# Kernel optimization log

Hardware: AMD Instinct MI355X
Metric: run time of the kernel (lower is better)

Reference implementation:

```python
import jax, jax.numpy as jnp
import numpy as np

N, E, F, H, C = 100000, 1600000, 128, 128, 40
NUM_LAYERS = 4
BN_EPS = 1e-5


def gcn_conv(x, src, dst, W, b, n):
    # PyG GCNConv with improved=True: self-loop edge weight 2.0
    e = src.shape[0]
    deg = jax.ops.segment_sum(jnp.ones((e,), x.dtype), dst, num_segments=n) + 2.0
    dinv = jnp.where(deg > 0, jax.lax.rsqrt(deg), 0.0)  # [n]
    xw = x @ W  # [n, out]
    coef = dinv[src] * dinv[dst]  # [e]
    agg = jax.ops.segment_sum(xw[src] * coef[:, None], dst, num_segments=n)
    agg = agg + (2.0 * dinv * dinv)[:, None] * xw  # self-loop term (weight 2)
    return agg + b


def batchnorm(x, gamma, beta):
    # training-mode BN (batch statistics, biased variance), eps=1e-5
    mu = jnp.mean(x, axis=0)
    var = jnp.mean(jnp.square(x - mu), axis=0)
    return (x - mu) * jax.lax.rsqrt(var + BN_EPS) * gamma + beta


def setup_inputs() -> dict:
    key = jax.random.key(0)
    ks = jax.random.split(key, 4)
    x = jax.random.normal(ks[0], (N, F), dtype=jnp.float32)
    edge_index = jax.random.randint(ks[1], (2, E), 0, N, dtype=jnp.int32)
    conv_w = jax.random.normal(ks[2], (NUM_LAYERS, F, H), dtype=jnp.float32) * 0.05
    conv_b = jnp.zeros((NUM_LAYERS, H), jnp.float32)
    bn_g = jnp.ones((NUM_LAYERS, H), jnp.float32)
    bn_b = jnp.zeros((NUM_LAYERS, H), jnp.float32)
    fc_w = jax.random.normal(ks[3], (NUM_LAYERS + 1, H, C), dtype=jnp.float32) * 0.05
    fc_b = jnp.zeros((NUM_LAYERS + 1, C), jnp.float32)
    return {"x": x, "edge_index": edge_index, "conv_w": conv_w, "conv_b": conv_b,
            "bn_g": bn_g, "bn_b": bn_b, "fc_w": fc_w, "fc_b": fc_b}


def reference(x, edge_index, conv_w, conv_b, bn_g, bn_b, fc_w, fc_b):
    n = x.shape[0]
    src, dst = edge_index[0], edge_index[1]
    outs = [x]
    h = x
    for i in range(NUM_LAYERS):
        h = gcn_conv(h, src, dst, conv_w[i], conv_b[i], n)
        h = batchnorm(h, bn_g[i], bn_b[i])
        h = jax.nn.relu(h)
        outs.append(h)
    # jumping-knowledge style sum of per-layer class heads (dropout = identity in eval)
    out = outs[0] @ fc_w[0] + fc_b[0]
    for i in range(1, NUM_LAYERS + 1):
        out = out + outs[i] @ fc_w[i] + fc_b[i]
    return jax.nn.log_softmax(out, axis=-1)
```

## Files before the change

kernel.cpp:

```cpp
#include <hip/hip_runtime.h>
#include <hip/hip_bf16.h>
#include <stdint.h>

#define NN 100000
#define NE 1600000
#define FD 128
#define CD 40
#define NL 4
#define NTB 391
#define TILE 4096
#define NTILES 391
#define EBCAP 8192
#define OCAP 5120

typedef __bf16 bf16;
typedef __bf16 bf16x8 __attribute__((ext_vector_type(8)));
typedef float f32x4 __attribute__((ext_vector_type(4)));

__device__ __forceinline__ unsigned short f2b(float f) {
  bf16 b = (bf16)f;
  unsigned short u;
  __builtin_memcpy(&u, &b, 2);
  return u;
}
__device__ __forceinline__ float lo16(unsigned int u) { return __uint_as_float(u << 16); }
__device__ __forceinline__ float hi16(unsigned int u) { return __uint_as_float(u & 0xffff0000u); }

__launch_bounds__(256)
__global__ void k_bfill(const int* __restrict__ src, const int* __restrict__ dst,
                        int* __restrict__ gcur, unsigned int* __restrict__ csrE) {
  __shared__ int cnt[NTB], pref[NTB], gofs[NTB];
  __shared__ int sc[512];
  __shared__ unsigned int stage[TILE];
  __shared__ unsigned short tgtb[TILE];
  int tid = threadIdx.x;
  int base = blockIdx.x * TILE;
  int tcnt = min(TILE, NE - base);
  for (int b = tid; b < NTB; b += 256) cnt[b] = 0;
  __syncthreads();
  unsigned int pay[16];
  int brk[16];
#pragma unroll
  for (int i = 0; i < 16; i++) {
    int e = base + tid + i * 256;
    if (e < NE) {
      int d = dst[e];
      int b = d >> 8;
      int r = atomicAdd(&cnt[b], 1);
      pay[i] = (unsigned int)src[e] | ((unsigned int)(d & 255) << 17);
      brk[i] = (b << 12) | r;
    } else {
      brk[i] = -1;
    }
  }
  __syncthreads();
  sc[tid] = (tid < NTB) ? cnt[tid] : 0;
  sc[tid + 256] = (tid + 256 < NTB) ? cnt[tid + 256] : 0;
  __syncthreads();
  for (int off = 1; off < 512; off <<= 1) {
    int a0 = (tid >= off) ? sc[tid - off] : 0;
    int a1 = sc[tid + 256 - off];
    __syncthreads();
    sc[tid] += a0;
    sc[tid + 256] += a1;
    __syncthreads();
  }
  for (int b = tid; b < NTB; b += 256) pref[b] = sc[b] - cnt[b];
  __syncthreads();
#pragma unroll
  for (int i = 0; i < 16; i++) {
    if (brk[i] >= 0) {
      int b = brk[i] >> 12, r = brk[i] & 4095;
      int p = pref[b] + r;
      if ((unsigned)p < (unsigned)TILE) {
        stage[p] = pay[i];
        tgtb[p] = (unsigned short)b;
      }
    }
  }
  for (int b = tid; b < NTB; b += 256) {
    int c = cnt[b];
    gofs[b] = c ? atomicAdd(&gcur[b], (c + 15) & ~15) : 0;
  }
  __syncthreads();
  for (int t = tid; t < tcnt; t += 256) {
    int b = tgtb[t];
    int pos = gofs[b] + (t - pref[b]);
    if ((unsigned)pos < (unsigned)EBCAP) csrE[(size_t)b * EBCAP + pos] = stage[t];
  }
  for (int b = tid; b < NTB; b += 256) {
    int c = cnt[b];
    if (c) {
      int pad = (c + 15) & ~15;
      for (int j = c; j < pad; j++) {
        int pos = gofs[b] + j;
        if ((unsigned)pos < (unsigned)EBCAP) csrE[(size_t)b * EBCAP + pos] = 0xFFFFFFFFu;
      }
    }
  }
}

__launch_bounds__(256)
__global__ void k_bsort(const int* __restrict__ gcur, const unsigned int* __restrict__ csrE,
                        unsigned int* __restrict__ csrp, float* __restrict__ dinv,
                        int2* __restrict__ rse) {
  __shared__ unsigned int ent[OCAP];
  __shared__ int c32[256], prefn[256], c2[256], sc[256];
  __shared__ int ecnt_s;
  int b = blockIdx.x, tid = threadIdx.x;
  c32[tid] = 0;
  c2[tid] = 0;
  if (tid == 0) ecnt_s = 0;
  __syncthreads();
  int claimed = min(gcur[b], EBCAP);
  const unsigned int* in = csrE + (size_t)b * EBCAP;
  for (int i = tid; i < claimed; i += 256) {
    unsigned int e = in[i];
    if (e != 0xFFFFFFFFu) {
      int idx = atomicAdd(&ecnt_s, 1);
      if (idx < OCAP) ent[idx] = e;
      atomicAdd(&c32[e >> 17], 1);
    }
  }
  __syncthreads();
  int cnt = min(ecnt_s, OCAP);
  int c = c32[tid];
  int pc = (c + 1) & ~1;
  sc[tid] = pc;
  __syncthreads();
  for (int off = 1; off < 256; off <<= 1) {
    int a = (tid >= off) ? sc[tid - off] : 0;
    __syncthreads();
    sc[tid] += a;
    __syncthreads();
  }
  prefn[tid] = sc[tid] - pc;
  int node = b * 256 + tid;
  if (node < NN) {
    dinv[node] = rsqrtf((float)c + 2.0f);
    int s = b * OCAP + prefn[tid];
    rse[node] = make_int2(s, s + pc);
  }
  if (c & 1) {
    int pos = prefn[tid] + c;
    if (pos < OCAP) csrp[b * OCAP + pos] = 0x1FFFFu;
  }
  __syncthreads();
  for (int i = tid; i < cnt; i += 256) {
    unsigned int e = ent[i];
    int dlo = e >> 17;
    int ofs = atomicAdd(&c2[dlo], 1);
    int pos = prefn[dlo] + ofs;
    if (pos < OCAP) csrp[b * OCAP + pos] = e & 0x1FFFFu;
  }
}

__global__ void k_pack(unsigned int* __restrict__ csrp, const float* __restrict__ dinv) {
  int i = blockIdx.x * 256 + threadIdx.x;
  unsigned int e = csrp[i];
  unsigned int s = e & 0x1FFFFu;
  unsigned int fix = 0;
  if (s < NN) {
    fix = (unsigned int)__float2uint_rn(dinv[s] * 32768.0f);
  } else {
    s = 0;
  }
  csrp[i] = (fix << 17) | s;
}

__global__ void k_repackall(const float* __restrict__ wc, const float* __restrict__ wf,
                            bf16* __restrict__ wp, bf16* __restrict__ wpfc) {
  int t = blockIdx.x * 256 + threadIdx.x;
  if (t < NL * 16384) {
    int j = t & 7, lane = (t >> 3) & 63, n0 = (t >> 9) & 7, k0 = (t >> 12) & 3, layer = t >> 14;
    int k = k0 * 32 + (lane >> 4) * 8 + j;
    int n = n0 * 16 + (lane & 15);
    wp[t] = (bf16)wc[(layer * 128 + k) * 128 + n];
    return;
  }
  t -= NL * 16384;
  if (t >= 5 * 6144) return;
  int j = t & 7, lane = (t >> 3) & 63;
  int rest = t >> 9;
  int n0 = rest % 3;
  int rest2 = rest / 3;
  int k0 = rest2 & 3, layer = rest2 >> 2;
  int k = k0 * 32 + (lane >> 4) * 8 + j;
  int n = n0 * 16 + (lane & 15);
  wpfc[t] = (n < CD) ? (bf16)wf[(layer * 128 + k) * CD + n] : (bf16)0.0f;
}

template <int NC, bool BN, bool INIT, bool LSM>
__launch_bounds__(256)
__global__ void k_gfc(const void* __restrict__ inp, const float* __restrict__ stats,
                      const float* __restrict__ g, const float* __restrict__ bb,
                      const bf16* __restrict__ wconv, const bf16* __restrict__ wfc,
                      const float* __restrict__ fcb, bf16* __restrict__ xwb,
                      float* __restrict__ out) {
  __shared__ bf16 wl[NC * 2048 + 6144];
  __shared__ float sc[128], sh[128];
  int tid = threadIdx.x;
  if (NC) {
    const uint4* gc = (const uint4*)wconv;
    uint4* lc = (uint4*)wl;
#pragma unroll
    for (int i = 0; i < NC; i++) lc[tid + i * 256] = gc[tid + i * 256];
  }
  {
    const uint4* gf = (const uint4*)wfc;
    uint4* lf = (uint4*)(wl + NC * 2048);
    for (int i = tid; i < 768; i += 256) lf[i] = gf[i];
  }
  if (BN && tid < 128) {
    const float invN = 1.0f / (float)NN;
    float s1 = stats[tid] + stats[256 + tid] + stats[512 + tid] + stats[768 + tid];
    float s2 = stats[128 + tid] + stats[384 + tid] + stats[640 + tid] + stats[896 + tid];
    float mu = s1 * invN;
    float var = s2 * invN - mu * mu;
    float s = g[tid] * rsqrtf(var + 1e-5f);
    sc[tid] = s;
    sh[tid] = bb[tid] - mu * s;
  }
  __syncthreads();
  int wid = tid >> 6, lane = tid & 63, quad = lane >> 4, l15 = lane & 15;
  int m_base = blockIdx.x * 64 + wid * 16;
  int arow = m_base + l15;
  if (arow >= NN) arow = NN - 1;
  f32x4 accc[NC > 0 ? NC : 1];
  f32x4 accf[3];
  if (NC) {
#pragma unroll
    for (int i = 0; i < NC; i++) accc[i] = (f32x4){0.f, 0.f, 0.f, 0.f};
  }
#pragma unroll
  for (int i = 0; i < 3; i++) accf[i] = (f32x4){0.f, 0.f, 0.f, 0.f};
#pragma unroll
  for (int k0 = 0; k0 < 4; k0++) {
    union Fr { bf16x8 v; unsigned short us[8]; } fr;
    if (BN) {
      const uint4* prow = (const uint4*)((const bf16*)inp + (size_t)arow * 128 + k0 * 32 + quad * 8);
      uint4 u = *prow;
      unsigned int uu[4] = {u.x, u.y, u.z, u.w};
      int kc = k0 * 32 + quad * 8;
#pragma unroll
      for (int p = 0; p < 4; p++) {
        float x0 = lo16(uu[p]) * sc[kc + 2 * p] + sh[kc + 2 * p];
        float x1 = hi16(uu[p]) * sc[kc + 2 * p + 1] + sh[kc + 2 * p + 1];
        fr.us[2 * p] = f2b(fmaxf(0.f, x0));
        fr.us[2 * p + 1] = f2b(fmaxf(0.f, x1));
      }
    } else {
      const float* prow = (const float*)inp + (size_t)arow * 128 + k0 * 32 + quad * 8;
      float4 u0 = *(const float4*)prow;
      float4 u1 = *(const float4*)(prow + 4);
      fr.us[0] = f2b(u0.x); fr.us[1] = f2b(u0.y); fr.us[2] = f2b(u0.z); fr.us[3] = f2b(u0.w);
      fr.us[4] = f2b(u1.x); fr.us[5] = f2b(u1.y); fr.us[6] = f2b(u1.z); fr.us[7] = f2b(u1.w);
    }
    bf16x8 a = fr.v;
    if (NC) {
#pragma unroll
      for (int n0 = 0; n0 < NC; n0++) {
        bf16x8 bfr = *reinterpret_cast<const bf16x8*>(&wl[(k0 * NC + n0) * 512 + lane * 8]);
        accc[n0] = __builtin_amdgcn_mfma_f32_16x16x32_bf16(a, bfr, accc[n0], 0, 0, 0);
      }
    }
#pragma unroll
    for (int n0 = 0; n0 < 3; n0++) {
      bf16x8 bfr = *reinterpret_cast<const bf16x8*>(&wl[NC * 2048 + (k0 * 3 + n0) * 512 + lane * 8]);
      accf[n0] = __builtin_amdgcn_mfma_f32_16x16x32_bf16(a, bfr, accf[n0], 0, 0, 0);
    }
  }
  int orow = m_base + quad * 4;
  if (NC) {
#pragma unroll
    for (int n0 = 0; n0 < NC; n0++) {
#pragma unroll
      for (int r2 = 0; r2 < 4; r2++) {
        int row = orow + r2;
        if (row < NN) xwb[(size_t)row * 128 + n0 * 16 + l15] = (bf16)accc[n0][r2];
      }
    }
  }
  if (!LSM) {
#pragma unroll
    for (int n0 = 0; n0 < 3; n0++) {
      int col = n0 * 16 + l15;
      if (col < CD) {
        float bias = fcb[col];
#pragma unroll
        for (int r2 = 0; r2 < 4; r2++) {
          int row = orow + r2;
          if (row < NN) {
            size_t idx = (size_t)row * CD + col;
            float v = accf[n0][r2] + bias;
            out[idx] = INIT ? v : out[idx] + v;
          }
        }
      }
    }
  } else {
    float bias[3];
#pragma unroll
    for (int n0 = 0; n0 < 3; n0++) {
      int col = n0 * 16 + l15;
      bias[n0] = (col < CD) ? fcb[col] : 0.f;
    }
#pragma unroll
    for (int r2 = 0; r2 < 4; r2++) {
      int row = orow + r2;
      float v[3];
#pragma unroll
      for (int n0 = 0; n0 < 3; n0++) {
        int col = n0 * 16 + l15;
        if (col < CD) {
          float prev = (row < NN) ? out[(size_t)row * CD + col] : 0.f;
          v[n0] = prev + accf[n0][r2] + bias[n0];
        } else {
          v[n0] = -1e30f;
        }
      }
      float m = fmaxf(v[0], fmaxf(v[1], v[2]));
#pragma unroll
      for (int s = 1; s < 16; s <<= 1) m = fmaxf(m, __shfl_xor(m, s, 64));
      float sum = 0.f;
#pragma unroll
      for (int n0 = 0; n0 < 3; n0++) {
        int col = n0 * 16 + l15;
        if (col < CD) sum += __expf(v[n0] - m);
      }
#pragma unroll
      for (int s = 1; s < 16; s <<= 1) sum += __shfl_xor(sum, s, 64);
      float ls = m + logf(sum);
      if (row < NN) {
#pragma unroll
        for (int n0 = 0; n0 < 3; n0++) {
          int col = n0 * 16 + l15;
          if (col < CD) out[(size_t)row * CD + col] = v[n0] - ls;
        }
      }
    }
  }
}

__launch_bounds__(256)
__global__ void k_gather(const uint2* __restrict__ xw, const int2* __restrict__ rse,
                         const unsigned int* __restrict__ csrp, const float* __restrict__ dinv,
                         uint2* __restrict__ aggb) {
  int tid = threadIdx.x;
  int n = blockIdx.x * 4 + (tid >> 6);
  int l = tid & 63;
  int h = l >> 5, cl = l & 31;
  float dn = dinv[n];
  float kk = dn * (1.0f / 32768.0f);
  uint2 u = xw[n * 32 + cl];
  float cs = (h == 0) ? 2.0f * dn * dn : 0.0f;
  float a0 = cs * lo16(u.x), a1 = cs * hi16(u.x);
  float a2 = cs * lo16(u.y), a3 = cs * hi16(u.y);
  int2 r = rse[n];
  int e = r.x, e1 = r.y;
  for (; e + 7 < e1; e += 8) {
    unsigned int p0 = csrp[e + h];
    unsigned int p1 = csrp[e + 2 + h];
    unsigned int p2 = csrp[e + 4 + h];
    unsigned int p3 = csrp[e + 6 + h];
    uint2 v0 = xw[(p0 & 0x1FFFFu) * 32 + cl];
    uint2 v1 = xw[(p1 & 0x1FFFFu) * 32 + cl];
    uint2 v2 = xw[(p2 & 0x1FFFFu) * 32 + cl];
    uint2 v3 = xw[(p3 & 0x1FFFFu) * 32 + cl];
    float c0 = (float)(p0 >> 17) * kk;
    float c1 = (float)(p1 >> 17) * kk;
    float c2 = (float)(p2 >> 17) * kk;
    float c3 = (float)(p3 >> 17) * kk;
    a0 += c0 * lo16(v0.x); a1 += c0 * hi16(v0.x); a2 += c0 * lo16(v0.y); a3 += c0 * hi16(v0.y);
    a0 += c1 * lo16(v1.x); a1 += c1 * hi16(v1.x); a2 += c1 * lo16(v1.y); a3 += c1 * hi16(v1.y);
    a0 += c2 * lo16(v2.x); a1 += c2 * hi16(v2.x); a2 += c2 * lo16(v2.y); a3 += c2 * hi16(v2.y);
    a0 += c3 * lo16(v3.x); a1 += c3 * hi16(v3.x); a2 += c3 * lo16(v3.y); a3 += c3 * hi16(v3.y);
  }
  for (; e + 1 < e1; e += 2) {
    unsigned int p0 = csrp[e + h];
    uint2 v0 = xw[(p0 & 0x1FFFFu) * 32 + cl];
    float c0 = (float)(p0 >> 17) * kk;
    a0 += c0 * lo16(v0.x); a1 += c0 * hi16(v0.x); a2 += c0 * lo16(v0.y); a3 += c0 * hi16(v0.y);
  }
  a0 += __shfl_xor(a0, 32, 64);
  a1 += __shfl_xor(a1, 32, 64);
  a2 += __shfl_xor(a2, 32, 64);
  a3 += __shfl_xor(a3, 32, 64);
  if (h == 0) {
    uint2 o;
    o.x = (unsigned int)f2b(a0) | ((unsigned int)f2b(a1) << 16);
    o.y = (unsigned int)f2b(a2) | ((unsigned int)f2b(a3) << 16);
    aggb[n * 32 + cl] = o;
  }
}

__launch_bounds__(256)
__global__ void k_stats(const uint2* __restrict__ agg, float* __restrict__ statsL) {
  __shared__ float ls1[128], ls2[128];
  int tid = threadIdx.x;
  if (tid < 128) { ls1[tid] = 0.f; ls2[tid] = 0.f; }
  __syncthreads();
  int cl = tid & 31, rg = tid >> 5;
  float s10 = 0.f, s11 = 0.f, s12 = 0.f, s13 = 0.f;
  float s20 = 0.f, s21 = 0.f, s22 = 0.f, s23 = 0.f;
  for (int r = blockIdx.x * 8 + rg; r < NN; r += 2048) {
    uint2 u = agg[r * 32 + cl];
    float b0 = lo16(u.x), b1 = hi16(u.x), b2 = lo16(u.y), b3 = hi16(u.y);
    s10 += b0; s20 += b0 * b0;
    s11 += b1; s21 += b1 * b1;
    s12 += b2; s22 += b2 * b2;
    s13 += b3; s23 += b3 * b3;
  }
  atomicAdd(&ls1[4 * cl + 0], s10);
  atomicAdd(&ls1[4 * cl + 1], s11);
  atomicAdd(&ls1[4 * cl + 2], s12);
  atomicAdd(&ls1[4 * cl + 3], s13);
  atomicAdd(&ls2[4 * cl + 0], s20);
  atomicAdd(&ls2[4 * cl + 1], s21);
  atomicAdd(&ls2[4 * cl + 2], s22);
  atomicAdd(&ls2[4 * cl + 3], s23);
  __syncthreads();
  if (tid < 128) {
    float* st = statsL + (blockIdx.x & 3) * 256;
    atomicAdd(&st[tid], ls1[tid]);
    atomicAdd(&st[128 + tid], ls2[tid]);
  }
}

static inline size_t alup(size_t x) { return (x + 255) & ~(size_t)255; }

extern "C" void kernel_launch(void* const* d_in, const int* in_sizes, int n_in,
                              void* d_out, int out_size, void* d_ws, size_t ws_size,
                              hipStream_t stream) {
  char* p = (char*)d_ws;
  bf16* xwb = (bf16*)p;     p += alup((size_t)NN * FD * 2);
  bf16* aggb = (bf16*)p;    p += alup((size_t)NN * FD * 2);
  float* dinv = (float*)p;  p += alup((size_t)NN * 4);
  int2* rse = (int2*)p;     p += alup((size_t)NN * 8);
  int* gcur = (int*)p;      p += alup((size_t)NTB * 4);
  unsigned int* csrE = (unsigned int*)p; p += alup((size_t)NTB * EBCAP * 4);
  unsigned int* csrp = (unsigned int*)p; p += alup((size_t)NTB * OCAP * 4);
  bf16* wp = (bf16*)p;      p += alup((size_t)NL * 16384 * 2);
  bf16* wpfc = (bf16*)p;    p += alup((size_t)5 * 6144 * 2);
  float* stats = (float*)p; p += alup((size_t)NL * 1024 * 4);

  const float* x = (const float*)d_in[0];
  const int* ei = (const int*)d_in[1];
  const int* srcv = ei;
  const int* dstv = ei + NE;
  const float* convw = (const float*)d_in[2];
  const float* bng = (const float*)d_in[4];
  const float* bnb = (const float*)d_in[5];
  const float* fcw = (const float*)d_in[6];
  const float* fcb = (const float*)d_in[7];
  float* out = (float*)d_out;

  hipMemsetAsync(gcur, 0, (size_t)NTB * sizeof(int), stream);
  hipMemsetAsync(stats, 0, (size_t)NL * 1024 * sizeof(float), stream);
  k_bfill<<<NTILES, 256, 0, stream>>>(srcv, dstv, gcur, csrE);
  k_bsort<<<NTB, 256, 0, stream>>>(gcur, csrE, csrp, dinv, rse);
  k_pack<<<NTB * OCAP / 256, 256, 0, stream>>>(csrp, dinv);
  k_repackall<<<(NL * 16384 + 5 * 6144 + 255) / 256, 256, 0, stream>>>(convw, fcw, wp, wpfc);

  k_gfc<8, false, true, false><<<1563, 256, 0, stream>>>(x, nullptr, nullptr, nullptr,
                                                         wp, wpfc, fcb, xwb, out);

  for (int L = 0; L < NL; L++) {
    k_gather<<<NN / 4, 256, 0, stream>>>((const uint2*)xwb, rse, csrp, dinv,
                                         (uint2*)aggb);
    float* st = stats + (size_t)L * 1024;
    k_stats<<<256, 256, 0, stream>>>((const uint2*)aggb, st);
    if (L < NL - 1) {
      k_gfc<8, true, false, false><<<1563, 256, 0, stream>>>(aggb, st, bng + L * FD, bnb + L * FD,
                                                             wp + (size_t)(L + 1) * 16384,
                                                             wpfc + (size_t)(L + 1) * 6144,
                                                             fcb + (L + 1) * CD, xwb, out);
    } else {
      k_gfc<0, true, false, true><<<1563, 256, 0, stream>>>(aggb, st, bng + L * FD, bnb + L * FD,
                                                            nullptr,
                                                            wpfc + (size_t)(L + 1) * 6144,
                                                            fcb + (L + 1) * CD, nullptr, out);
    }
  }
}
```

Before: 599.0 us.

## Split gather feature halves by XCD with persistent work-queue blocks

The gather is now a persistent kernel. Blocks claim 64-node chunks from two atomic work queues, and the queue is chosen by the XCD id parity, so each group of XCDs mostly touches one 64-column half of xw. That keeps a smaller working set in each XCD's L2. Each wave processes 16 nodes, with four 16-lane groups splitting the edges, and CSR rows are padded to multiples of 4 to match. The trade-offs are atomic contention on the queues, extra padding work, and reliance on hardware XCD register behaviour.

Result: slower. 959.6 us (+60.2%).

```diff
diff --git a/kernel.cpp b/kernel.cpp
--- a/kernel.cpp
+++ b/kernel.cpp
@@ -12,6 +12,7 @@
 #define NTILES 391
 #define EBCAP 8192
 #define OCAP 5120
+#define CPH 1563
 
 typedef __bf16 bf16;
 typedef __bf16 bf16x8 __attribute__((ext_vector_type(8)));
@@ -125,7 +126,7 @@
   __syncthreads();
   int cnt = min(ecnt_s, OCAP);
   int c = c32[tid];
-  int pc = (c + 1) & ~1;
+  int pc = (c + 3) & ~3;
   sc[tid] = pc;
   __syncthreads();
   for (int off = 1; off < 256; off <<= 1) {
@@ -141,8 +142,8 @@
     int s = b * OCAP + prefn[tid];
     rse[node] = make_int2(s, s + pc);
   }
-  if (c & 1) {
-    int pos = prefn[tid] + c;
+  for (int j = c; j < pc; j++) {
+    int pos = prefn[tid] + j;
     if (pos < OCAP) csrp[b * OCAP + pos] = 0x1FFFFu;
   }
   __syncthreads();
@@ -345,52 +346,72 @@
 __launch_bounds__(256)
 __global__ void k_gather(const uint2* __restrict__ xw, const int2* __restrict__ rse,
                          const unsigned int* __restrict__ csrp, const float* __restrict__ dinv,
-                         uint2* __restrict__ aggb) {
+                         uint2* __restrict__ aggb, int* __restrict__ wq) {
+  __shared__ int sh_g;
   int tid = threadIdx.x;
-  int n = blockIdx.x * 4 + (tid >> 6);
-  int l = tid & 63;
-  int h = l >> 5, cl = l & 31;
-  float dn = dinv[n];
-  float kk = dn * (1.0f / 32768.0f);
-  uint2 u = xw[n * 32 + cl];
-  float cs = (h == 0) ? 2.0f * dn * dn : 0.0f;
-  float a0 = cs * lo16(u.x), a1 = cs * hi16(u.x);
-  float a2 = cs * lo16(u.y), a3 = cs * hi16(u.y);
-  int2 r = rse[n];
-  int e = r.x, e1 = r.y;
-  for (; e + 7 < e1; e += 8) {
-    unsigned int p0 = csrp[e + h];
-    unsigned int p1 = csrp[e + 2 + h];
-    unsigned int p2 = csrp[e + 4 + h];
-    unsigned int p3 = csrp[e + 6 + h];
-    uint2 v0 = xw[(p0 & 0x1FFFFu) * 32 + cl];
-    uint2 v1 = xw[(p1 & 0x1FFFFu) * 32 + cl];
-    uint2 v2 = xw[(p2 & 0x1FFFFu) * 32 + cl];
-    uint2 v3 = xw[(p3 & 0x1FFFFu) * 32 + cl];
-    float c0 = (float)(p0 >> 17) * kk;
-    float c1 = (float)(p1 >> 17) * kk;
-    float c2 = (float)(p2 >> 17) * kk;
-    float c3 = (float)(p3 >> 17) * kk;
-    a0 += c0 * lo16(v0.x); a1 += c0 * hi16(v0.x); a2 += c0 * lo16(v0.y); a3 += c0 * hi16(v0.y);
-    a0 += c1 * lo16(v1.x); a1 += c1 * hi16(v1.x); a2 += c1 * lo16(v1.y); a3 += c1 * hi16(v1.y);
-    a0 += c2 * lo16(v2.x); a1 += c2 * hi16(v2.x); a2 += c2 * lo16(v2.y); a3 += c2 * hi16(v2.y);
-    a0 += c3 * lo16(v3.x); a1 += c3 * hi16(v3.x); a2 += c3 * lo16(v3.y); a3 += c3 * hi16(v3.y);
-  }
-  for (; e + 1 < e1; e += 2) {
-    unsigned int p0 = csrp[e + h];
-    uint2 v0 = xw[(p0 & 0x1FFFFu) * 32 + cl];
-    float c0 = (float)(p0 >> 17) * kk;
-    a0 += c0 * lo16(v0.x); a1 += c0 * hi16(v0.x); a2 += c0 * lo16(v0.y); a3 += c0 * hi16(v0.y);
-  }
-  a0 += __shfl_xor(a0, 32, 64);
-  a1 += __shfl_xor(a1, 32, 64);
-  a2 += __shfl_xor(a2, 32, 64);
-  a3 += __shfl_xor(a3, 32, 64);
-  if (h == 0) {
-    uint2 o;
-    o.x = (unsigned int)f2b(a0) | ((unsigned int)f2b(a1) << 16);
-    o.y = (unsigned int)f2b(a2) | ((unsigned int)f2b(a3) << 16);
-    aggb[n * 32 + cl] = o;
+  unsigned int xcd;
+  asm volatile("s_getreg_b32 %0, hwreg(HW_REG_XCC_ID)" : "=s"(xcd));
+  int myhalf = (int)(xcd & 1);
+  int wave = tid >> 6, lane = tid & 63;
+  int h = lane >> 4, cl = lane & 15;
+  for (;;) {
+    if (tid == 0) {
+      int g = atomicAdd(&wq[myhalf], 1);
+      int hf = myhalf;
+      if (g >= CPH) {
+        g = atomicAdd(&wq[1 - myhalf], 1);
+        hf = 1 - myhalf;
+      }
+      sh_g = (g >= CPH) ? -1 : (g | (hf << 16));
+    }
+    __syncthreads();
+    int enc = sh_g;
+    __syncthreads();
+    if (enc < 0) break;
+    int chunk = enc & 0xFFFF;
+    int hofs = (enc >> 16) << 4;
+    int nbase = chunk * 64 + wave * 16;
+    for (int i = 0; i < 16; i++) {
+      int n = nbase + i;
+      if (n >= NN) break;
+      float dn = dinv[n];
+      float kk = dn * (1.0f / 32768.0f);
+      uint2 u = xw[n * 32 + hofs + cl];
+      float cs = (h == 0) ? 2.0f * dn * dn : 0.0f;
+      float a0 = cs * lo16(u.x), a1 = cs * hi16(u.x);
+      float a2 = cs * lo16(u.y), a3 = cs * hi16(u.y);
+      int2 r = rse[n];
+      int e = r.x, e1 = r.y;
+      for (; e + 7 < e1; e += 8) {
+        unsigned int p0 = csrp[e + h];
+        unsigned int p1 = csrp[e + 4 + h];
+        uint2 v0 = xw[(p0 & 0x1FFFFu) * 32 + hofs + cl];
+        uint2 v1 = xw[(p1 & 0x1FFFFu) * 32 + hofs + cl];
+        float c0 = (float)(p0 >> 17) * kk;
+        float c1 = (float)(p1 >> 17) * kk;
+        a0 += c0 * lo16(v0.x); a1 += c0 * hi16(v0.x);
+        a2 += c0 * lo16(v0.y); a3 += c0 * hi16(v0.y);
+        a0 += c1 * lo16(v1.x); a1 += c1 * hi16(v1.x);
+        a2 += c1 * lo16(v1.y); a3 += c1 * hi16(v1.y);
+      }
+      if (e < e1) {
+        unsigned int p0 = csrp[e + h];
+        uint2 v0 = xw[(p0 & 0x1FFFFu) * 32 + hofs + cl];
+        float c0 = (float)(p0 >> 17) * kk;
+        a0 += c0 * lo16(v0.x); a1 += c0 * hi16(v0.x);
+        a2 += c0 * lo16(v0.y); a3 += c0 * hi16(v0.y);
+      }
+      a0 += __shfl_xor(a0, 16, 64); a0 += __shfl_xor(a0, 32, 64);
+      a1 += __shfl_xor(a1, 16, 64); a1 += __shfl_xor(a1, 32, 64);
+      a2 += __shfl_xor(a2, 16, 64); a2 += __shfl_xor(a2, 32, 64);
+      a3 += __shfl_xor(a3, 16, 64); a3 += __shfl_xor(a3, 32, 64);
+      if (h == 0) {
+        uint2 o;
+        o.x = (unsigned int)f2b(a0) | ((unsigned int)f2b(a1) << 16);
+        o.y = (unsigned int)f2b(a2) | ((unsigned int)f2b(a3) << 16);
+        aggb[n * 32 + hofs + cl] = o;
+      }
+    }
   }
 }
 
@@ -443,6 +464,7 @@
   bf16* wp = (bf16*)p;      p += alup((size_t)NL * 16384 * 2);
   bf16* wpfc = (bf16*)p;    p += alup((size_t)5 * 6144 * 2);
   float* stats = (float*)p; p += alup((size_t)NL * 1024 * 4);
+  int* wq = (int*)p;        p += alup((size_t)NL * 2 * 4);
 
   const float* x = (const float*)d_in[0];
   const int* ei = (const int*)d_in[1];
@@ -457,6 +479,7 @@
 
   hipMemsetAsync(gcur, 0, (size_t)NTB * sizeof(int), stream);
   hipMemsetAsync(stats, 0, (size_t)NL * 1024 * sizeof(float), stream);
+  hipMemsetAsync(wq, 0, (size_t)NL * 2 * sizeof(int), stream);
   k_bfill<<<NTILES, 256, 0, stream>>>(srcv, dstv, gcur, csrE);
   k_bsort<<<NTB, 256, 0, stream>>>(gcur, csrE, csrp, dinv, rse);
   k_pack<<<NTB * OCAP / 256, 256, 0, stream>>>(csrp, dinv);
@@ -466,8 +489,8 @@
                                                          wp, wpfc, fcb, xwb, out);
 
   for (int L = 0; L < NL; L++) {
-    k_gather<<<NN / 4, 256, 0, stream>>>((const uint2*)xwb, rse, csrp, dinv,
-                                         (uint2*)aggb);
+    k_gather<<<1024, 256, 0, stream>>>((const uint2*)xwb, rse, csrp, dinv,
+                                       (uint2*)aggb, wq + L * 2);
     float* st = stats + (size_t)L * 1024;
     k_stats<<<256, 256, 0, stream>>>((const uint2*)aggb, st);
     if (L < NL - 1) {
```
